# Kernel optimization log

Measured on AMD Instinct MI355X. Metric: run time of the kernel, lower is better.

## Reference

```python
import jax, jax.numpy as jnp
import numpy as np

B, N, E, K = 4, 40000, 240000, 128
C_IN, C_W, C_OUT, N_BLOCK = 6, 128, 3, 4


def setup_inputs() -> dict:
    key = jax.random.key(0)
    ks = jax.random.split(key, 20)
    s = lambda k, sh, fan: jax.random.normal(k, sh, jnp.float32) / np.sqrt(fan).astype(np.float32)
    inp = {}
    inp["x_in"] = jax.random.normal(ks[0], (B, N, C_IN), jnp.float32)
    inp["mass"] = jax.random.uniform(ks[1], (B, N), jnp.float32) + 0.1  # positive lumped mass
    inp["evals"] = jax.random.uniform(ks[2], (B, K), jnp.float32) * 10.0  # nonneg Laplacian eigenvalues
    inp["evecs"] = jax.random.normal(ks[3], (B, N, K), jnp.float32) / np.float32(np.sqrt(N))
    inp["rows"] = jax.random.randint(ks[4], (E,), 0, N, jnp.int32)
    inp["cols"] = jax.random.randint(ks[5], (E,), 0, N, jnp.int32)
    inp["gradX_vals"] = jax.random.normal(ks[6], (B, E), jnp.float32)
    inp["gradY_vals"] = jax.random.normal(ks[7], (B, E), jnp.float32)
    inp["w_first"] = s(ks[8], (C_IN, C_W), C_IN)
    inp["b_first"] = jnp.zeros((C_W,), jnp.float32)
    inp["diff_time"] = jax.random.uniform(ks[9], (N_BLOCK, C_W), jnp.float32) * 0.1 + 1e-4  # learned times, clamped positive
    inp["A_re"] = s(ks[10], (N_BLOCK, C_W, C_W), C_W)
    inp["A_im"] = s(ks[11], (N_BLOCK, C_W, C_W), C_W)
    inp["mlp_w0"] = s(ks[12], (N_BLOCK, 3 * C_W, C_W), 3 * C_W)
    inp["mlp_b0"] = jnp.zeros((N_BLOCK, C_W), jnp.float32)
    inp["mlp_w1"] = s(ks[13], (N_BLOCK, C_W, C_W), C_W)
    inp["mlp_b1"] = jnp.zeros((N_BLOCK, C_W), jnp.float32)
    inp["mlp_w2"] = s(ks[14], (N_BLOCK, C_W, C_W), C_W)
    inp["mlp_b2"] = jnp.zeros((N_BLOCK, C_W), jnp.float32)
    inp["w_last"] = s(ks[15], (C_W, C_OUT), C_W)
    inp["b_last"] = jnp.zeros((C_OUT,), jnp.float32)
    return inp


def reference(x_in, mass, evals, evecs, rows, cols, gradX_vals, gradY_vals,
              w_first, b_first, diff_time, A_re, A_im,
              mlp_w0, mlp_b0, mlp_w1, mlp_b1, mlp_w2, mlp_b2, w_last, b_last):
    def spmm(vals, x):
        # sparse [N,N] COO (shared pattern, per-sample vals) @ dense [N,C]
        return jax.ops.segment_sum(vals[:, None] * x[cols], rows, num_segments=N)

    x = x_in @ w_first + b_first  # [B,N,C_W]
    for i in range(N_BLOCK):
        # --- LearnedTimeDiffusion (spectral) ---
        x_spec = jnp.einsum('bnk,bnc->bkc', evecs, x * mass[..., None])  # [B,K,C]
        coefs = jnp.exp(-evals[:, :, None] * diff_time[i][None, None, :])  # [B,K,C]
        x_diffuse = jnp.einsum('bnk,bkc->bnc', evecs, coefs * x_spec)  # [B,N,C]
        # --- per-sample sparse gradient operators (the batched torch.mm loop) ---
        gX = jax.vmap(spmm)(gradX_vals, x_diffuse)  # [B,N,C]
        gY = jax.vmap(spmm)(gradY_vals, x_diffuse)  # [B,N,C]
        # --- SpatialGradientFeatures with learned rotations (complex multiply) ---
        Breal = gX @ A_re[i] - gY @ A_im[i]
        Bimag = gY @ A_re[i] + gX @ A_im[i]
        grad_feat = jnp.tanh(gX * Breal + gY * Bimag)  # [B,N,C]
        # --- MiniMLP + residual ---
        feat = jnp.concatenate([x, x_diffuse, grad_feat], axis=-1)  # [B,N,3C]
        h = jax.nn.relu(feat @ mlp_w0[i] + mlp_b0[i])
        h = jax.nn.relu(h @ mlp_w1[i] + mlp_b1[i])
        h = h @ mlp_w2[i] + mlp_b2[i]
        x = h + x
    return x @ w_last + b_last  # [B,N,C_OUT]
```

## Files before the change

### kernel.cpp

```cpp
#include <hip/hip_runtime.h>

#define B_ 4
#define N_ 40000
#define E_ 240000
#define NB_SCAN ((N_ + 255) / 256)

typedef unsigned short u16;
typedef unsigned int u32;
typedef __attribute__((ext_vector_type(8))) short bf16x8;
typedef __attribute__((ext_vector_type(4))) float f32x4;

__device__ __forceinline__ float b2f(u16 h) {
    u32 u = ((u32)h) << 16;
    return __uint_as_float(u);
}
__device__ __forceinline__ u16 f2b(float f) {
    u32 u = __float_as_uint(f);
    u32 r = (u + 0x7fffu + ((u >> 16) & 1u)) >> 16;
    return (u16)r;
}

__global__ __launch_bounds__(256) void first_linear_kern(
    const float* __restrict__ x_in, const float* __restrict__ w,
    const float* __restrict__ bias, u16* __restrict__ xout, int M)
{
    __shared__ float sw[6 * 128];
    __shared__ float sb[128];
    int t = threadIdx.x;
    for (int i = t; i < 768; i += 256) sw[i] = w[i];
    if (t < 128) sb[t] = bias[t];
    __syncthreads();
    int idx = blockIdx.x * 256 + t;
    int row = idx >> 4;
    int cg = (idx & 15) * 8;
    if (row >= M) return;
    const float* xr = x_in + (size_t)row * 6;
    float xv[6];
#pragma unroll
    for (int j = 0; j < 6; j++) xv[j] = xr[j];
    float acc[8];
#pragma unroll
    for (int i = 0; i < 8; i++) acc[i] = sb[cg + i];
#pragma unroll
    for (int j = 0; j < 6; j++)
#pragma unroll
        for (int i = 0; i < 8; i++) acc[i] += xv[j] * sw[j * 128 + cg + i];
    ushort4 h0, h1;
    h0.x = f2b(acc[0]); h0.y = f2b(acc[1]); h0.z = f2b(acc[2]); h0.w = f2b(acc[3]);
    h1.x = f2b(acc[4]); h1.y = f2b(acc[5]); h1.z = f2b(acc[6]); h1.w = f2b(acc[7]);
    uint4 pk;
    pk.x = (u32)h0.x | ((u32)h0.y << 16);
    pk.y = (u32)h0.z | ((u32)h0.w << 16);
    pk.z = (u32)h1.x | ((u32)h1.y << 16);
    pk.w = (u32)h1.z | ((u32)h1.w << 16);
    *(uint4*)(xout + (size_t)row * 128 + cg) = pk;
}

__global__ __launch_bounds__(256) void pack_w_kern(
    const float* __restrict__ src, u16* __restrict__ dst, int K)
{
    int i = blockIdx.z;
    src += (size_t)i * K * 128;
    dst += (size_t)i * K * 128;
    int idx = blockIdx.x * 256 + threadIdx.x;
    int n = idx / K;
    int k = idx % K;
    dst[idx] = f2b(src[(size_t)k * 128 + n]);
}

__global__ __launch_bounds__(256) void pack_rot_kern(
    const float* __restrict__ Are, const float* __restrict__ Aim,
    u16* __restrict__ WR1, u16* __restrict__ WR2)
{
    int i = blockIdx.z;
    const float* are = Are + (size_t)i * 16384;
    const float* aim = Aim + (size_t)i * 16384;
    int idx = blockIdx.x * 256 + threadIdx.x;
    int n = idx >> 8;
    int k = idx & 255;
    float v1, v2;
    if (k < 128) { float a = are[(size_t)k * 128 + n]; v1 = a; v2 = a; }
    else         { float a = aim[(size_t)(k - 128) * 128 + n]; v1 = -a; v2 = a; }
    WR1[(size_t)i * 32768 + idx] = f2b(v1);
    WR2[(size_t)i * 32768 + idx] = f2b(v2);
}

__global__ __launch_bounds__(256) void hist_kern(const int* __restrict__ rows, int* count)
{
    int e = blockIdx.x * 256 + threadIdx.x;
    if (e < E_) atomicAdd(&count[rows[e]], 1);
}

__device__ __forceinline__ int block_incl_scan_256(int v, int t)
{
    __shared__ int wsum[4];
    int lane = t & 63;
    int wid = t >> 6;
    int x = v;
#pragma unroll
    for (int off = 1; off < 64; off <<= 1) {
        int y = __shfl_up(x, off);
        if (lane >= off) x += y;
    }
    if (lane == 63) wsum[wid] = x;
    __syncthreads();
    if (t == 0) {
        int s = 0;
#pragma unroll
        for (int i = 0; i < 4; i++) { int tm = wsum[i]; wsum[i] = s; s += tm; }
    }
    __syncthreads();
    return x + wsum[wid];
}

__global__ __launch_bounds__(256) void scan1_kern(
    const int* __restrict__ count, int* __restrict__ excl_out,
    int* __restrict__ blockTotals)
{
    int t = threadIdx.x;
    int g = blockIdx.x * 256 + t;
    int v = (g < N_) ? count[g] : 0;
    int incl = block_incl_scan_256(v, t);
    if (g < N_) excl_out[g] = incl - v;
    if (t == 255) blockTotals[blockIdx.x] = incl;
}

__global__ __launch_bounds__(256) void scan2_kern(
    const int* __restrict__ blockTotals, int* __restrict__ blockOffs,
    int* __restrict__ totalOut)
{
    int t = threadIdx.x;
    int v = (t < NB_SCAN) ? blockTotals[t] : 0;
    int incl = block_incl_scan_256(v, t);
    if (t < NB_SCAN) blockOffs[t] = incl - v;
    if (t == 255) *totalOut = incl;
}

__global__ __launch_bounds__(256) void scan3_kern(
    int* __restrict__ rowptr, int* __restrict__ nextp,
    const int* __restrict__ blockOffs)
{
    int t = threadIdx.x;
    int g = blockIdx.x * 256 + t;
    if (g >= N_) return;
    int v = rowptr[g] + blockOffs[blockIdx.x];
    rowptr[g] = v;
    nextp[g] = v;
}

__global__ __launch_bounds__(256) void scatter_idx_kern(
    const int* __restrict__ rows, const int* __restrict__ cols,
    int* nextp, int* __restrict__ scols, int* __restrict__ sperm)
{
    int e = blockIdx.x * 256 + threadIdx.x;
    if (e >= E_) return;
    int r = rows[e];
    int pos = atomicAdd(&nextp[r], 1);
    scols[pos] = cols[e];
    sperm[pos] = e;
}

__global__ __launch_bounds__(256) void gather_vals_kern(
    const int* __restrict__ sperm,
    const float* __restrict__ gvx, const float* __restrict__ gvy,
    float* __restrict__ svx, float* __restrict__ svy)
{
    int pos = blockIdx.x * 256 + threadIdx.x;
    if (pos >= E_) return;
    int e = sperm[pos];
#pragma unroll
    for (int b = 0; b < B_; b++) {
        svx[(size_t)b * E_ + pos] = gvx[(size_t)b * E_ + e];
        svy[(size_t)b * E_ + pos] = gvy[(size_t)b * E_ + e];
    }
}

__global__ __launch_bounds__(256) void spmm_csr_kern(
    const int* __restrict__ rowptr, const int* __restrict__ scols,
    const float* __restrict__ svx, const float* __restrict__ svy,
    const u16* __restrict__ xd, u16* __restrict__ gXY0, u16* __restrict__ gXY1)
{
    const size_t NZ = (size_t)N_ * 128;
    int z = blockIdx.z;
    const float* svx_b = svx + (size_t)z * E_;
    const float* svy_b = svy + (size_t)z * E_;
    const u16* xd_b = xd + (size_t)z * NZ;
    u16* base = (z < 2) ? (gXY0 + (size_t)z * 2 * NZ) : (gXY1 + (size_t)(z - 2) * 2 * NZ);
    u16* gXh = base;
    u16* gYh = base + NZ;

    int t = threadIdx.x;
    int r = blockIdx.x * 4 + (t >> 6);
    int c2 = (t & 63) * 2;
    int beg = rowptr[r], end = rowptr[r + 1];
    float ax0 = 0.f, ax1 = 0.f, ay0 = 0.f, ay1 = 0.f;
    int j = beg;
    for (; j + 1 < end; j += 2) {
        int ca = scols[j], cb = scols[j + 1];
        u32 xwa = *(const u32*)(xd_b + (size_t)ca * 128 + c2);
        u32 xwb = *(const u32*)(xd_b + (size_t)cb * 128 + c2);
        float vxa = svx_b[j], vya = svy_b[j];
        float vxb = svx_b[j + 1], vyb = svy_b[j + 1];
        float xa0 = b2f((u16)(xwa & 0xffffu)), xa1 = b2f((u16)(xwa >> 16));
        float xb0 = b2f((u16)(xwb & 0xffffu)), xb1 = b2f((u16)(xwb >> 16));
        ax0 += vxa * xa0; ax1 += vxa * xa1;
        ay0 += vya * xa0; ay1 += vya * xa1;
        ax0 += vxb * xb0; ax1 += vxb * xb1;
        ay0 += vyb * xb0; ay1 += vyb * xb1;
    }
    if (j < end) {
        int col = scols[j];
        u32 xw = *(const u32*)(xd_b + (size_t)col * 128 + c2);
        float x0 = b2f((u16)(xw & 0xffffu));
        float x1 = b2f((u16)(xw >> 16));
        float vx = svx_b[j], vy = svy_b[j];
        ax0 += vx * x0; ax1 += vx * x1;
        ay0 += vy * x0; ay1 += vy * x1;
    }
    u32 px = (u32)f2b(ax0) | ((u32)f2b(ax1) << 16);
    u32 py = (u32)f2b(ay0) | ((u32)f2b(ay1) << 16);
    *(u32*)(gXh + (size_t)r * 128 + c2) = px;
    *(u32*)(gYh + (size_t)r * 128 + c2) = py;
}

__global__ __launch_bounds__(256) void spec_stage1_mfma_kern(
    const u16* __restrict__ x, const float* __restrict__ mass,
    const float* __restrict__ evecs, float* __restrict__ partials)
{
    __shared__ __align__(16) u16 sEVh[128][40];
    __shared__ __align__(16) u16 sEVl[128][40];
    __shared__ __align__(16) u16 sXM[128][40];
    int b = blockIdx.y;
    int pb = blockIdx.x;
    const u16* xb = x + (size_t)b * N_ * 128;
    const float* mb = mass + (size_t)b * N_;
    const float* eb = evecs + (size_t)b * N_ * 128;
    float* dst = partials + ((size_t)b * 128 + pb) * 16384;

    int t = threadIdx.x;
    int wv = t >> 6;
    int lane = t & 63;
    int quad = lane >> 4;
    int r16 = lane & 15;
    int kb = wv * 32;
    int kc = (t & 63) * 2;
    int nh = wv;

    f32x4 acc[2][8];
#pragma unroll
    for (int i = 0; i < 2; i++)
#pragma unroll
        for (int j = 0; j < 8; j++) acc[i][j] = (f32x4){0.f, 0.f, 0.f, 0.f};

    for (int ch = pb; ch < N_ / 32; ch += 128) {
        int nbase = ch * 32 + nh * 8;
        float4 m0 = *(const float4*)(mb + nbase);
        float4 m1 = *(const float4*)(mb + nbase + 4);
        float mm[8] = {m0.x, m0.y, m0.z, m0.w, m1.x, m1.y, m1.z, m1.w};
        u32 eh0[4], eh1[4], el0[4], el1[4], xq0[4], xq1[4];
#pragma unroll
        for (int jp = 0; jp < 4; jp++) {
            eh0[jp] = 0; eh1[jp] = 0; el0[jp] = 0;
            el1[jp] = 0; xq0[jp] = 0; xq1[jp] = 0;
        }
#pragma unroll
        for (int j = 0; j < 8; j++) {
            float2 e = *(const float2*)(eb + (size_t)(nbase + j) * 128 + kc);
            u32 xw = *(const u32*)(xb + (size_t)(nbase + j) * 128 + kc);
            u16 h0 = f2b(e.x);
            u16 h1 = f2b(e.y);
            u16 l0 = f2b(e.x - b2f(h0));
            u16 l1 = f2b(e.y - b2f(h1));
            u16 q0 = f2b(b2f((u16)(xw & 0xffffu)) * mm[j]);
            u16 q1 = f2b(b2f((u16)(xw >> 16)) * mm[j]);
            int sh = (j & 1) * 16;
            int jp = j >> 1;
            eh0[jp] |= ((u32)h0) << sh; eh1[jp] |= ((u32)h1) << sh;
            el0[jp] |= ((u32)l0) << sh; el1[jp] |= ((u32)l1) << sh;
            xq0[jp] |= ((u32)q0) << sh; xq1[jp] |= ((u32)q1) << sh;
        }
        __syncthreads();
        *(uint4*)&sEVh[kc][nh * 8]     = make_uint4(eh0[0], eh0[1], eh0[2], eh0[3]);
        *(uint4*)&sEVh[kc + 1][nh * 8] = make_uint4(eh1[0], eh1[1], eh1[2], eh1[3]);
        *(uint4*)&sEVl[kc][nh * 8]     = make_uint4(el0[0], el0[1], el0[2], el0[3]);
        *(uint4*)&sEVl[kc + 1][nh * 8] = make_uint4(el1[0], el1[1], el1[2], el1[3]);
        *(uint4*)&sXM[kc][nh * 8]      = make_uint4(xq0[0], xq0[1], xq0[2], xq0[3]);
        *(uint4*)&sXM[kc + 1][nh * 8]  = make_uint4(xq1[0], xq1[1], xq1[2], xq1[3]);
        __syncthreads();

        bf16x8 ah0 = *(const bf16x8*)&sEVh[kb + r16][quad * 8];
        bf16x8 ah1 = *(const bf16x8*)&sEVh[kb + 16 + r16][quad * 8];
        bf16x8 al0 = *(const bf16x8*)&sEVl[kb + r16][quad * 8];
        bf16x8 al1 = *(const bf16x8*)&sEVl[kb + 16 + r16][quad * 8];
#pragma unroll
        for (int nt = 0; nt < 8; nt++) {
            bf16x8 bx = *(const bf16x8*)&sXM[nt * 16 + r16][quad * 8];
            acc[0][nt] = __builtin_amdgcn_mfma_f32_16x16x32_bf16(ah0, bx, acc[0][nt], 0, 0, 0);
            acc[1][nt] = __builtin_amdgcn_mfma_f32_16x16x32_bf16(ah1, bx, acc[1][nt], 0, 0, 0);
            acc[0][nt] = __builtin_amdgcn_mfma_f32_16x16x32_bf16(al0, bx, acc[0][nt], 0, 0, 0);
            acc[1][nt] = __builtin_amdgcn_mfma_f32_16x16x32_bf16(al1, bx, acc[1][nt], 0, 0, 0);
        }
    }

#pragma unroll
    for (int mt = 0; mt < 2; mt++)
#pragma unroll
        for (int nt = 0; nt < 8; nt++)
#pragma unroll
            for (int reg = 0; reg < 4; reg++) {
                int kk = kb + mt * 16 + quad * 4 + reg;
                int cc = nt * 16 + r16;
                dst[(size_t)kk * 128 + cc] = acc[mt][nt][reg];
            }
}

__global__ __launch_bounds__(128) void spec_stage2_coef_kern(
    const float* __restrict__ partials, const float* __restrict__ evals,
    const float* __restrict__ dt, u16* __restrict__ ys_t)
{
    int b = blockIdx.x >> 7;
    int k = blockIdx.x & 127;
    int c = threadIdx.x;
    const float* p = partials + (size_t)b * 128 * 16384 + (size_t)k * 128 + c;
    float s = 0.f;
#pragma unroll 8
    for (int pb = 0; pb < 128; pb++) s += p[(size_t)pb * 16384];
    float co = expf(-evals[b * 128 + k] * dt[c]);
    ys_t[((size_t)b * 128 + c) * 128 + k] = f2b(s * co);
}

template <int KK, bool AF32>
__global__ __launch_bounds__(256) void mgemm_kern(
    const void* __restrict__ A0v,
    const u16* __restrict__ Wp, u16* __restrict__ outp,
    size_t aBatch, size_t wBatch, size_t oBatch)
{
    __shared__ u16 sA[64][72];
    __shared__ u16 sB[128][72];
    int z = blockIdx.z;
    const u16* Wb = Wp + wBatch * (size_t)z;
    size_t aOff = aBatch * (size_t)z;
    size_t oOff = oBatch * (size_t)z;

    int t = threadIdx.x;
    int m0 = blockIdx.x * 64;
    int wv = t >> 6;
    int lane = t & 63;
    int quad = lane >> 4;
    int r16 = lane & 15;
    int mw = (wv & 1) * 32;
    int nw = (wv >> 1) * 64;

    f32x4 acc[2][4];
#pragma unroll
    for (int i = 0; i < 2; i++)
#pragma unroll
        for (int j = 0; j < 4; j++) acc[i][j] = (f32x4){0.f, 0.f, 0.f, 0.f};

#pragma unroll 1
    for (int kt = 0; kt < KK / 64; kt++) {
        int kbase = kt * 64;
        __syncthreads();
        if (AF32) {
            const float* Af = (const float*)A0v + aOff;
#pragma unroll
            for (int p = 0; p < 4; p++) {
                int idx = p * 256 + t;
                int row = idx >> 4;
                int seg = idx & 15;
                float4 v = *(const float4*)(Af + (size_t)(m0 + row) * 128 + kbase + seg * 4);
                ushort4 h;
                h.x = f2b(v.x); h.y = f2b(v.y); h.z = f2b(v.z); h.w = f2b(v.w);
                *(ushort4*)&sA[row][seg * 4] = h;
            }
        } else {
            const u16* Ah = (const u16*)A0v + aOff;
#pragma unroll
            for (int p = 0; p < 2; p++) {
                int idx = p * 256 + t;
                int row = idx >> 3;
                int seg = idx & 7;
                *(uint4*)&sA[row][seg * 8] =
                    *(const uint4*)(Ah + (size_t)(m0 + row) * 128 + kbase + seg * 8);
            }
        }
        {
#pragma unroll
            for (int p = 0; p < 4; p++) {
                int idx = p * 256 + t;
                int n = idx >> 3;
                int seg = idx & 7;
                *(uint4*)&sB[n][seg * 8] =
                    *(const uint4*)(Wb + (size_t)n * KK + kbase + seg * 8);
            }
        }
        __syncthreads();

#pragma unroll
        for (int ks = 0; ks < 2; ks++) {
            int ko = ks * 32 + quad * 8;
            bf16x8 a0 = *(const bf16x8*)&sA[mw + r16][ko];
            bf16x8 a1 = *(const bf16x8*)&sA[mw + 16 + r16][ko];
            bf16x8 b0 = *(const bf16x8*)&sB[nw + r16][ko];
            bf16x8 b1 = *(const bf16x8*)&sB[nw + 16 + r16][ko];
            bf16x8 b2 = *(const bf16x8*)&sB[nw + 32 + r16][ko];
            bf16x8 b3 = *(const bf16x8*)&sB[nw + 48 + r16][ko];
            acc[0][0] = __builtin_amdgcn_mfma_f32_16x16x32_bf16(a0, b0, acc[0][0], 0, 0, 0);
            acc[0][1] = __builtin_amdgcn_mfma_f32_16x16x32_bf16(a0, b1, acc[0][1], 0, 0, 0);
            acc[0][2] = __builtin_amdgcn_mfma_f32_16x16x32_bf16(a0, b2, acc[0][2], 0, 0, 0);
            acc[0][3] = __builtin_amdgcn_mfma_f32_16x16x32_bf16(a0, b3, acc[0][3], 0, 0, 0);
            acc[1][0] = __builtin_amdgcn_mfma_f32_16x16x32_bf16(a1, b0, acc[1][0], 0, 0, 0);
            acc[1][1] = __builtin_amdgcn_mfma_f32_16x16x32_bf16(a1, b1, acc[1][1], 0, 0, 0);
            acc[1][2] = __builtin_amdgcn_mfma_f32_16x16x32_bf16(a1, b2, acc[1][2], 0, 0, 0);
            acc[1][3] = __builtin_amdgcn_mfma_f32_16x16x32_bf16(a1, b3, acc[1][3], 0, 0, 0);
        }
    }

#pragma unroll
    for (int nt = 0; nt < 4; nt++) {
        int col = nw + nt * 16 + r16;
#pragma unroll
        for (int mt = 0; mt < 2; mt++) {
#pragma unroll
            for (int reg = 0; reg < 4; reg++) {
                int row = m0 + mw + mt * 16 + quad * 4 + reg;
                outp[oOff + (size_t)row * 128 + col] = f2b(acc[mt][nt][reg]);
            }
        }
    }
}

__global__ __launch_bounds__(512) void mlp_rot_fused_kern(
    const u16* __restrict__ xg, const u16* __restrict__ xdg,
    const u16* __restrict__ gXY0, const u16* __restrict__ gXY1,
    const u16* __restrict__ WR1, const u16* __restrict__ WR2,
    const u16* __restrict__ W0, const u16* __restrict__ W1, const u16* __restrict__ W2,
    const float* __restrict__ b0, const float* __restrict__ b1, const float* __restrict__ b2,
    u16* __restrict__ outp)
{
    __shared__ u16 sGX[64][136];
    __shared__ u16 sGY[64][136];
    __shared__ u16 sB[128][72];
    __shared__ __align__(16) u16 sHbuf[9728];
    __shared__ u16 sA[64][72];
#define HV(r, c) sHbuf[(r) * 152 + (c)]
#define WV(n, c) sHbuf[(n) * 72 + (c)]

    const size_t NZ = (size_t)N_ * 128;
    int z = blockIdx.z;
    const u16* gX = (z < 2) ? (gXY0 + (size_t)z * 2 * NZ) : (gXY1 + (size_t)(z - 2) * 2 * NZ);
    const u16* gY = gX + NZ;
    int m0n = blockIdx.x * 64;
    size_t growBase = ((size_t)z * N_ + m0n) * 128;

    int t = threadIdx.x;
    int wv = t >> 6;
    int lane = t & 63;
    int quad = lane >> 4;
    int r16 = lane & 15;
    int mw = (wv & 1) * 32;
    int nw = (wv >> 1) * 32;

#pragma unroll
    for (int p = 0; p < 2; p++) {
        int idx = p * 512 + t;
        int row = idx >> 4;
        int seg = idx & 15;
        *(uint4*)&sGX[row][seg * 8] = *(const uint4*)(gX + (size_t)(m0n + row) * 128 + seg * 8);
        *(uint4*)&sGY[row][seg * 8] = *(const uint4*)(gY + (size_t)(m0n + row) * 128 + seg * 8);
    }

    f32x4 accRe[2][2], accIm[2][2];
#pragma unroll
    for (int i = 0; i < 2; i++)
#pragma unroll
        for (int j = 0; j < 2; j++) {
            accRe[i][j] = (f32x4){0.f, 0.f, 0.f, 0.f};
            accIm[i][j] = (f32x4){0.f, 0.f, 0.f, 0.f};
        }

#pragma unroll 1
    for (int c = 0; c < 4; c++) {
        __syncthreads();
#pragma unroll
        for (int p = 0; p < 2; p++) {
            int idx = p * 512 + t;
            int n = idx >> 3;
            int seg = idx & 7;
            *(uint4*)&sB[n][seg * 8] = *(const uint4*)(WR1 + (size_t)n * 256 + c * 64 + seg * 8);
            *(uint4*)&WV(n, seg * 8) = *(const uint4*)(WR2 + (size_t)n * 256 + c * 64 + seg * 8);
        }
        __syncthreads();

        const u16 (*sRe)[136] = (c < 2) ? sGX : sGY;
        const u16 (*sIm)[136] = (c < 2) ? sGY : sGX;
        int kob = (c & 1) * 64;
#pragma unroll
        for (int ks = 0; ks < 2; ks++) {
            int ko = kob + ks * 32 + quad * 8;
            int kb = ks * 32 + quad * 8;
            bf16x8 aRe0 = *(const bf16x8*)&sRe[mw + r16][ko];
            bf16x8 aRe1 = *(const bf16x8*)&sRe[mw + 16 + r16][ko];
            bf16x8 aIm0 = *(const bf16x8*)&sIm[mw + r16][ko];
            bf16x8 aIm1 = *(const bf16x8*)&sIm[mw + 16 + r16][ko];
#pragma unroll
            for (int j = 0; j < 2; j++) {
                bf16x8 w1f = *(const bf16x8*)&sB[nw + 16 * j + r16][kb];
                bf16x8 w2f = *(const bf16x8*)&WV(nw + 16 * j + r16, kb);
                accRe[0][j] = __builtin_amdgcn_mfma_f32_16x16x32_bf16(aRe0, w1f, accRe[0][j], 0, 0, 0);
                accRe[1][j] = __builtin_amdgcn_mfma_f32_16x16x32_bf16(aRe1, w1f, accRe[1][j], 0, 0, 0);
                accIm[0][j] = __builtin_amdgcn_mfma_f32_16x16x32_bf16(aIm0, w2f, accIm[0][j], 0, 0, 0);
                accIm[1][j] = __builtin_amdgcn_mfma_f32_16x16x32_bf16(aIm1, w2f, accIm[1][j], 0, 0, 0);
            }
        }
    }

    __syncthreads();
#pragma unroll
    for (int nt = 0; nt < 2; nt++) {
        int col = nw + nt * 16 + r16;
#pragma unroll
        for (int mt = 0; mt < 2; mt++)
#pragma unroll
            for (int reg = 0; reg < 4; reg++) {
                int lrow = mw + mt * 16 + quad * 4 + reg;
                float gx = b2f(sGX[lrow][col]);
                float gy = b2f(sGY[lrow][col]);
                float v = tanhf(gx * accRe[mt][nt][reg] + gy * accIm[mt][nt][reg]);
                sGX[lrow][col] = f2b(v);
            }
    }

    f32x4 acc[2][2];
#pragma unroll
    for (int i = 0; i < 2; i++)
#pragma unroll
        for (int j = 0; j < 2; j++) acc[i][j] = (f32x4){0.f, 0.f, 0.f, 0.f};
#pragma unroll 1
    for (int kt = 0; kt < 6; kt++) {
        int kbase = kt * 64;
        int kloc = kbase & 127;
        __syncthreads();
        if (kt < 4) {
            const u16* Ap = (kt < 2) ? xg : xdg;
            {
                int row = t >> 3;
                int seg = t & 7;
                *(uint4*)&sA[row][seg * 8] =
                    *(const uint4*)(Ap + growBase + (size_t)row * 128 + kloc + seg * 8);
            }
        }
#pragma unroll
        for (int p = 0; p < 2; p++) {
            int idx = p * 512 + t;
            int n = idx >> 3;
            int seg = idx & 7;
            *(uint4*)&sB[n][seg * 8] = *(const uint4*)(W0 + (size_t)n * 384 + kbase + seg * 8);
        }
        __syncthreads();
#pragma unroll
        for (int ks = 0; ks < 2; ks++) {
            int ko = ks * 32 + quad * 8;
            bf16x8 a0, a1;
            if (kt < 4) {
                a0 = *(const bf16x8*)&sA[mw + r16][ko];
                a1 = *(const bf16x8*)&sA[mw + 16 + r16][ko];
            } else {
                a0 = *(const bf16x8*)&sGX[mw + r16][kloc + ko];
                a1 = *(const bf16x8*)&sGX[mw + 16 + r16][kloc + ko];
            }
#pragma unroll
            for (int j = 0; j < 2; j++) {
                bf16x8 bj = *(const bf16x8*)&sB[nw + 16 * j + r16][ko];
                acc[0][j] = __builtin_amdgcn_mfma_f32_16x16x32_bf16(a0, bj, acc[0][j], 0, 0, 0);
                acc[1][j] = __builtin_amdgcn_mfma_f32_16x16x32_bf16(a1, bj, acc[1][j], 0, 0, 0);
            }
        }
    }
    __syncthreads();
#pragma unroll
    for (int nt = 0; nt < 2; nt++) {
        int col = nw + nt * 16 + r16;
        float bv = b0[col];
#pragma unroll
        for (int mt = 0; mt < 2; mt++)
#pragma unroll
            for (int reg = 0; reg < 4; reg++) {
                int rl = mw + mt * 16 + quad * 4 + reg;
                HV(rl, col) = f2b(fmaxf(acc[mt][nt][reg] + bv, 0.f));
            }
    }

#pragma unroll
    for (int i = 0; i < 2; i++)
#pragma unroll
        for (int j = 0; j < 2; j++) acc[i][j] = (f32x4){0.f, 0.f, 0.f, 0.f};
#pragma unroll 1
    for (int kt = 0; kt < 2; kt++) {
        int kbase = kt * 64;
        __syncthreads();
#pragma unroll
        for (int p = 0; p < 2; p++) {
            int idx = p * 512 + t;
            int n = idx >> 3;
            int seg = idx & 7;
            *(uint4*)&sB[n][seg * 8] = *(const uint4*)(W1 + (size_t)n * 128 + kbase + seg * 8);
        }
        __syncthreads();
#pragma unroll
        for (int ks = 0; ks < 2; ks++) {
            int ko = kbase + ks * 32 + quad * 8;
            int kb = ks * 32 + quad * 8;
            bf16x8 a0 = *(const bf16x8*)&HV(mw + r16, ko);
            bf16x8 a1 = *(const bf16x8*)&HV(mw + 16 + r16, ko);
#pragma unroll
            for (int j = 0; j < 2; j++) {
                bf16x8 bj = *(const bf16x8*)&sB[nw + 16 * j + r16][kb];
                acc[0][j] = __builtin_amdgcn_mfma_f32_16x16x32_bf16(a0, bj, acc[0][j], 0, 0, 0);
                acc[1][j] = __builtin_amdgcn_mfma_f32_16x16x32_bf16(a1, bj, acc[1][j], 0, 0, 0);
            }
        }
    }
    __syncthreads();
#pragma unroll
    for (int nt = 0; nt < 2; nt++) {
        int col = nw + nt * 16 + r16;
        float bv = b1[col];
#pragma unroll
        for (int mt = 0; mt < 2; mt++)
#pragma unroll
            for (int reg = 0; reg < 4; reg++) {
                int rl = mw + mt * 16 + quad * 4 + reg;
                HV(rl, col) = f2b(fmaxf(acc[mt][nt][reg] + bv, 0.f));
            }
    }

#pragma unroll
    for (int i = 0; i < 2; i++)
#pragma unroll
        for (int j = 0; j < 2; j++) acc[i][j] = (f32x4){0.f, 0.f, 0.f, 0.f};
#pragma unroll 1
    for (int kt = 0; kt < 2; kt++) {
        int kbase = kt * 64;
        __syncthreads();
#pragma unroll
        for (int p = 0; p < 2; p++) {
            int idx = p * 512 + t;
            int n = idx >> 3;
            int seg = idx & 7;
            *(uint4*)&sB[n][seg * 8] = *(const uint4*)(W2 + (size_t)n * 128 + kbase + seg * 8);
        }
        __syncthreads();
#pragma unroll
        for (int ks = 0; ks < 2; ks++) {
            int ko = kbase + ks * 32 + quad * 8;
            int kb = ks * 32 + quad * 8;
            bf16x8 a0 = *(const bf16x8*)&HV(mw + r16, ko);
            bf16x8 a1 = *(const bf16x8*)&HV(mw + 16 + r16, ko);
#pragma unroll
            for (int j = 0; j < 2; j++) {
                bf16x8 bj = *(const bf16x8*)&sB[nw + 16 * j + r16][kb];
                acc[0][j] = __builtin_amdgcn_mfma_f32_16x16x32_bf16(a0, bj, acc[0][j], 0, 0, 0);
                acc[1][j] = __builtin_amdgcn_mfma_f32_16x16x32_bf16(a1, bj, acc[1][j], 0, 0, 0);
            }
        }
    }
#pragma unroll
    for (int nt = 0; nt < 2; nt++) {
        int col = nw + nt * 16 + r16;
        float bv = b2[col];
#pragma unroll
        for (int mt = 0; mt < 2; mt++)
#pragma unroll
            for (int reg = 0; reg < 4; reg++) {
                int row = mw + mt * 16 + quad * 4 + reg;
                float v = acc[mt][nt][reg] + bv + b2f(xg[growBase + (size_t)row * 128 + col]);
                outp[growBase + (size_t)row * 128 + col] = f2b(v);
            }
    }
#undef HV
#undef WV
}

__global__ __launch_bounds__(256) void last_linear_kern(
    const u16* __restrict__ x, const float* __restrict__ w,
    const float* __restrict__ bias, float* __restrict__ outp, int M)
{
    __shared__ float sw[128 * 3];
    int t = threadIdx.x;
    for (int i = t; i < 384; i += 256) sw[i] = w[i];
    __syncthreads();
    int wave = t >> 6;
    int lane = t & 63;
    int row = blockIdx.x * 4 + wave;
    if (row >= M) return;
    const u16* xr = x + (size_t)row * 128;
    float p0 = 0.f, p1 = 0.f, p2 = 0.f;
#pragma unroll
    for (int h = 0; h < 2; h++) {
        int c = lane + h * 64;
        float xv = b2f(xr[c]);
        p0 += xv * sw[c * 3 + 0];
        p1 += xv * sw[c * 3 + 1];
        p2 += xv * sw[c * 3 + 2];
    }
#pragma unroll
    for (int off = 32; off > 0; off >>= 1) {
        p0 += __shfl_xor(p0, off);
        p1 += __shfl_xor(p1, off);
        p2 += __shfl_xor(p2, off);
    }
    if (lane == 0) {
        float* o = outp + (size_t)row * 3;
        o[0] = p0 + bias[0];
        o[1] = p1 + bias[1];
        o[2] = p2 + bias[2];
    }
}

extern "C" void kernel_launch(void* const* d_in, const int* in_sizes, int n_in,
                              void* d_out, int out_size, void* d_ws, size_t ws_size,
                              hipStream_t stream)
{
    const float* x_in    = (const float*)d_in[0];
    const float* mass    = (const float*)d_in[1];
    const float* evals   = (const float*)d_in[2];
    const float* evecs   = (const float*)d_in[3];
    const int*   rows    = (const int*)  d_in[4];
    const int*   cols    = (const int*)  d_in[5];
    const float* gvx     = (const float*)d_in[6];
    const float* gvy     = (const float*)d_in[7];
    const float* w_first = (const float*)d_in[8];
    const float* b_first = (const float*)d_in[9];
    const float* dtimes  = (const float*)d_in[10];
    const float* A_re    = (const float*)d_in[11];
    const float* A_im    = (const float*)d_in[12];
    const float* w0      = (const float*)d_in[13];
    const float* b0      = (const float*)d_in[14];
    const float* w1      = (const float*)d_in[15];
    const float* b1      = (const float*)d_in[16];
    const float* w2      = (const float*)d_in[17];
    const float* b2      = (const float*)d_in[18];
    const float* w_last  = (const float*)d_in[19];
    const float* b_last  = (const float*)d_in[20];
    float* outp = (float*)d_out;

    const size_t SZ = (size_t)B_ * N_ * 128;
    const size_t NZ = (size_t)N_ * 128;

    u16* P0 = (u16*)d_ws;
    u16* P1 = P0 + SZ;
    u16* GF = P1 + SZ;
    float* SC = (float*)(GF + SZ);
    u16* ys_t = (u16*)(SC + 8388608);
    u16* WP0 = (u16*)(SC + 2 * NZ);
    u16* WP1 = WP0 + 4 * 49152;
    u16* WP2 = WP1 + 4 * 16384;
    u16* WR1 = WP2 + 4 * 16384;
    u16* WR2 = WR1 + 4 * 32768;
    int* rowptr = (int*)(WR2 + 4 * 32768);
    int* nextp  = rowptr + 40004;
    int* scols  = nextp + N_;
    float* svx  = (float*)(scols + E_);
    float* svy  = svx + (size_t)B_ * E_;

    u16* x  = P0;
    u16* xd = P1;
    const int M = B_ * N_;

    int* bTot  = (int*)SC;
    int* bOff  = bTot + 512;
    int* sperm = bTot + 1024;
    hipMemsetAsync(nextp, 0, N_ * sizeof(int), stream);
    hist_kern<<<dim3((E_ + 255) / 256), 256, 0, stream>>>(rows, nextp);
    scan1_kern<<<dim3(NB_SCAN), 256, 0, stream>>>(nextp, rowptr, bTot);
    scan2_kern<<<dim3(1), 256, 0, stream>>>(bTot, bOff, rowptr + N_);
    scan3_kern<<<dim3(NB_SCAN), 256, 0, stream>>>(rowptr, nextp, bOff);
    scatter_idx_kern<<<dim3((E_ + 255) / 256), 256, 0, stream>>>(
        rows, cols, nextp, scols, sperm);
    gather_vals_kern<<<dim3((E_ + 255) / 256), 256, 0, stream>>>(
        sperm, gvx, gvy, svx, svy);

    pack_w_kern<<<dim3(192, 1, 4), 256, 0, stream>>>(w0, WP0, 384);
    pack_w_kern<<<dim3(64, 1, 4), 256, 0, stream>>>(w1, WP1, 128);
    pack_w_kern<<<dim3(64, 1, 4), 256, 0, stream>>>(w2, WP2, 128);
    pack_rot_kern<<<dim3(128, 1, 4), 256, 0, stream>>>(A_re, A_im, WR1, WR2);

    first_linear_kern<<<dim3(M * 16 / 256), 256, 0, stream>>>(x_in, w_first, b_first, x, M);

    u16* GXY0 = GF;
    u16* GXY1 = (u16*)SC;

    for (int i = 0; i < 4; i++) {
        spec_stage1_mfma_kern<<<dim3(128, B_), 256, 0, stream>>>(x, mass, evecs, SC);
        spec_stage2_coef_kern<<<dim3(B_ * 128), 128, 0, stream>>>(
            SC, evals, dtimes + (size_t)i * 128, ys_t);
        mgemm_kern<128, true><<<dim3(N_ / 64, 1, B_), 256, 0, stream>>>(
            evecs, ys_t, xd, NZ, (size_t)128 * 128, NZ);
        spmm_csr_kern<<<dim3(N_ / 4, 1, B_), 256, 0, stream>>>(
            rowptr, scols, svx, svy, xd, GXY0, GXY1);
        mlp_rot_fused_kern<<<dim3(N_ / 64, 1, B_), 512, 0, stream>>>(
            x, xd, GXY0, GXY1,
            WR1 + (size_t)i * 32768, WR2 + (size_t)i * 32768,
            WP0 + (size_t)i * 49152, WP1 + (size_t)i * 16384, WP2 + (size_t)i * 16384,
            b0 + (size_t)i * 128, b1 + (size_t)i * 128, b2 + (size_t)i * 128,
            xd);
        u16* tmp = x; x = xd; xd = tmp;
    }

    last_linear_kern<<<dim3(M / 4), 256, 0, stream>>>(x, w_last, b_last, outp, M);
}
```

Before: 1.209 ms.

## Load MFMA operands directly from global memory instead of staging through LDS

The diffuse GEMM and the fused rotation/MLP kernel now feed MFMA fragments straight from global memory (evecs converted to bf16 in registers, weights read per lane). This drops the shared-memory staging and most of the block-wide barriers. Shared memory use falls to the gradient tiles plus one hidden buffer, which may raise occupancy. The cost is uncoalesced, redundant global reads of the weight and activation fragments that now depend on L1/L2 hits.

Result: slower. 1.681 ms (+39.1%).

```diff
diff --git a/kernel.cpp b/kernel.cpp
--- a/kernel.cpp
+++ b/kernel.cpp
@@ -18,6 +18,14 @@
     u32 u = __float_as_uint(f);
     u32 r = (u + 0x7fffu + ((u >> 16) & 1u)) >> 16;
     return (u16)r;
+}
+__device__ __forceinline__ bf16x8 ld8f(const float* p) {
+    float4 v0 = *(const float4*)p;
+    float4 v1 = *(const float4*)(p + 4);
+    union { bf16x8 v; u16 s[8]; } u;
+    u.s[0] = f2b(v0.x); u.s[1] = f2b(v0.y); u.s[2] = f2b(v0.z); u.s[3] = f2b(v0.w);
+    u.s[4] = f2b(v1.x); u.s[5] = f2b(v1.y); u.s[6] = f2b(v1.z); u.s[7] = f2b(v1.w);
+    return u.v;
 }
 
 __global__ __launch_bounds__(256) void first_linear_kern(
@@ -329,18 +337,15 @@
     ys_t[((size_t)b * 128 + c) * 128 + k] = f2b(s * co);
 }
 
-template <int KK, bool AF32>
-__global__ __launch_bounds__(256) void mgemm_kern(
-    const void* __restrict__ A0v,
-    const u16* __restrict__ Wp, u16* __restrict__ outp,
-    size_t aBatch, size_t wBatch, size_t oBatch)
-{
-    __shared__ u16 sA[64][72];
-    __shared__ u16 sB[128][72];
+__global__ __launch_bounds__(256) void diffuse_gemm_kern(
+    const float* __restrict__ evecs, const u16* __restrict__ ys_t,
+    u16* __restrict__ xd)
+{
+    const size_t NZ = (size_t)N_ * 128;
     int z = blockIdx.z;
-    const u16* Wb = Wp + wBatch * (size_t)z;
-    size_t aOff = aBatch * (size_t)z;
-    size_t oOff = oBatch * (size_t)z;
+    const float* eb = evecs + (size_t)z * NZ;
+    const u16* yb = ys_t + (size_t)z * 16384;
+    u16* ob = xd + (size_t)z * NZ;
 
     int t = threadIdx.x;
     int m0 = blockIdx.x * 64;
@@ -357,62 +362,25 @@
 #pragma unroll
         for (int j = 0; j < 4; j++) acc[i][j] = (f32x4){0.f, 0.f, 0.f, 0.f};
 
-#pragma unroll 1
-    for (int kt = 0; kt < KK / 64; kt++) {
-        int kbase = kt * 64;
-        __syncthreads();
-        if (AF32) {
-            const float* Af = (const float*)A0v + aOff;
-#pragma unroll
-            for (int p = 0; p < 4; p++) {
-                int idx = p * 256 + t;
-                int row = idx >> 4;
-                int seg = idx & 15;
-                float4 v = *(const float4*)(Af + (size_t)(m0 + row) * 128 + kbase + seg * 4);
-                ushort4 h;
-                h.x = f2b(v.x); h.y = f2b(v.y); h.z = f2b(v.z); h.w = f2b(v.w);
-                *(ushort4*)&sA[row][seg * 4] = h;
-            }
-        } else {
-            const u16* Ah = (const u16*)A0v + aOff;
-#pragma unroll
-            for (int p = 0; p < 2; p++) {
-                int idx = p * 256 + t;
-                int row = idx >> 3;
-                int seg = idx & 7;
-                *(uint4*)&sA[row][seg * 8] =
-                    *(const uint4*)(Ah + (size_t)(m0 + row) * 128 + kbase + seg * 8);
-            }
-        }
-        {
-#pragma unroll
-            for (int p = 0; p < 4; p++) {
-                int idx = p * 256 + t;
-                int n = idx >> 3;
-                int seg = idx & 7;
-                *(uint4*)&sB[n][seg * 8] =
-                    *(const uint4*)(Wb + (size_t)n * KK + kbase + seg * 8);
-            }
-        }
-        __syncthreads();
-
+#pragma unroll
+    for (int kt = 0; kt < 2; kt++) {
 #pragma unroll
         for (int ks = 0; ks < 2; ks++) {
-            int ko = ks * 32 + quad * 8;
-            bf16x8 a0 = *(const bf16x8*)&sA[mw + r16][ko];
-            bf16x8 a1 = *(const bf16x8*)&sA[mw + 16 + r16][ko];
-            bf16x8 b0 = *(const bf16x8*)&sB[nw + r16][ko];
-            bf16x8 b1 = *(const bf16x8*)&sB[nw + 16 + r16][ko];
-            bf16x8 b2 = *(const bf16x8*)&sB[nw + 32 + r16][ko];
-            bf16x8 b3 = *(const bf16x8*)&sB[nw + 48 + r16][ko];
+            int ko = kt * 64 + ks * 32 + quad * 8;
+            bf16x8 a0 = ld8f(eb + (size_t)(m0 + mw + r16) * 128 + ko);
+            bf16x8 a1 = ld8f(eb + (size_t)(m0 + mw + 16 + r16) * 128 + ko);
+            bf16x8 b0 = *(const bf16x8*)(yb + (size_t)(nw + r16) * 128 + ko);
+            bf16x8 b1 = *(const bf16x8*)(yb + (size_t)(nw + 16 + r16) * 128 + ko);
+            bf16x8 b2v = *(const bf16x8*)(yb + (size_t)(nw + 32 + r16) * 128 + ko);
+            bf16x8 b3v = *(const bf16x8*)(yb + (size_t)(nw + 48 + r16) * 128 + ko);
             acc[0][0] = __builtin_amdgcn_mfma_f32_16x16x32_bf16(a0, b0, acc[0][0], 0, 0, 0);
             acc[0][1] = __builtin_amdgcn_mfma_f32_16x16x32_bf16(a0, b1, acc[0][1], 0, 0, 0);
-            acc[0][2] = __builtin_amdgcn_mfma_f32_16x16x32_bf16(a0, b2, acc[0][2], 0, 0, 0);
-            acc[0][3] = __builtin_amdgcn_mfma_f32_16x16x32_bf16(a0, b3, acc[0][3], 0, 0, 0);
+            acc[0][2] = __builtin_amdgcn_mfma_f32_16x16x32_bf16(a0, b2v, acc[0][2], 0, 0, 0);
+            acc[0][3] = __builtin_amdgcn_mfma_f32_16x16x32_bf16(a0, b3v, acc[0][3], 0, 0, 0);
             acc[1][0] = __builtin_amdgcn_mfma_f32_16x16x32_bf16(a1, b0, acc[1][0], 0, 0, 0);
             acc[1][1] = __builtin_amdgcn_mfma_f32_16x16x32_bf16(a1, b1, acc[1][1], 0, 0, 0);
-            acc[1][2] = __builtin_amdgcn_mfma_f32_16x16x32_bf16(a1, b2, acc[1][2], 0, 0, 0);
-            acc[1][3] = __builtin_amdgcn_mfma_f32_16x16x32_bf16(a1, b3, acc[1][3], 0, 0, 0);
+            acc[1][2] = __builtin_amdgcn_mfma_f32_16x16x32_bf16(a1, b2v, acc[1][2], 0, 0, 0);
+            acc[1][3] = __builtin_amdgcn_mfma_f32_16x16x32_bf16(a1, b3v, acc[1][3], 0, 0, 0);
         }
     }
 
@@ -424,7 +392,7 @@
 #pragma unroll
             for (int reg = 0; reg < 4; reg++) {
                 int row = m0 + mw + mt * 16 + quad * 4 + reg;
-                outp[oOff + (size_t)row * 128 + col] = f2b(acc[mt][nt][reg]);
+                ob[(size_t)row * 128 + col] = f2b(acc[mt][nt][reg]);
             }
         }
     }
@@ -440,11 +408,7 @@
 {
     __shared__ u16 sGX[64][136];
     __shared__ u16 sGY[64][136];
-    __shared__ u16 sB[128][72];
-    __shared__ __align__(16) u16 sHbuf[9728];
-    __shared__ u16 sA[64][72];
-#define HV(r, c) sHbuf[(r) * 152 + (c)]
-#define WV(n, c) sHbuf[(n) * 72 + (c)]
+    __shared__ u16 sH[64][136];
 
     const size_t NZ = (size_t)N_ * 128;
     int z = blockIdx.z;
@@ -469,6 +433,7 @@
         *(uint4*)&sGX[row][seg * 8] = *(const uint4*)(gX + (size_t)(m0n + row) * 128 + seg * 8);
         *(uint4*)&sGY[row][seg * 8] = *(const uint4*)(gY + (size_t)(m0n + row) * 128 + seg * 8);
     }
+    __syncthreads();
 
     f32x4 accRe[2][2], accIm[2][2];
 #pragma unroll
@@ -479,34 +444,24 @@
             accIm[i][j] = (f32x4){0.f, 0.f, 0.f, 0.f};
         }
 
-#pragma unroll 1
+#pragma unroll
     for (int c = 0; c < 4; c++) {
-        __syncthreads();
-#pragma unroll
-        for (int p = 0; p < 2; p++) {
-            int idx = p * 512 + t;
-            int n = idx >> 3;
-            int seg = idx & 7;
-            *(uint4*)&sB[n][seg * 8] = *(const uint4*)(WR1 + (size_t)n * 256 + c * 64 + seg * 8);
-            *(uint4*)&WV(n, seg * 8) = *(const uint4*)(WR2 + (size_t)n * 256 + c * 64 + seg * 8);
-        }
-        __syncthreads();
-
         const u16 (*sRe)[136] = (c < 2) ? sGX : sGY;
         const u16 (*sIm)[136] = (c < 2) ? sGY : sGX;
         int kob = (c & 1) * 64;
 #pragma unroll
         for (int ks = 0; ks < 2; ks++) {
             int ko = kob + ks * 32 + quad * 8;
-            int kb = ks * 32 + quad * 8;
+            int wk = c * 64 + ks * 32 + quad * 8;
             bf16x8 aRe0 = *(const bf16x8*)&sRe[mw + r16][ko];
             bf16x8 aRe1 = *(const bf16x8*)&sRe[mw + 16 + r16][ko];
             bf16x8 aIm0 = *(const bf16x8*)&sIm[mw + r16][ko];
             bf16x8 aIm1 = *(const bf16x8*)&sIm[mw + 16 + r16][ko];
 #pragma unroll
             for (int j = 0; j < 2; j++) {
-                bf16x8 w1f = *(const bf16x8*)&sB[nw + 16 * j + r16][kb];
-                bf16x8 w2f = *(const bf16x8*)&WV(nw + 16 * j + r16, kb);
+                int n = nw + 16 * j + r16;
+                bf16x8 w1f = *(const bf16x8*)(WR1 + (size_t)n * 256 + wk);
+                bf16x8 w2f = *(const bf16x8*)(WR2 + (size_t)n * 256 + wk);
                 accRe[0][j] = __builtin_amdgcn_mfma_f32_16x16x32_bf16(aRe0, w1f, accRe[0][j], 0, 0, 0);
                 accRe[1][j] = __builtin_amdgcn_mfma_f32_16x16x32_bf16(aRe1, w1f, accRe[1][j], 0, 0, 0);
                 accIm[0][j] = __builtin_amdgcn_mfma_f32_16x16x32_bf16(aIm0, w2f, accIm[0][j], 0, 0, 0);
@@ -530,54 +485,38 @@
                 sGX[lrow][col] = f2b(v);
             }
     }
+    __syncthreads();
 
     f32x4 acc[2][2];
 #pragma unroll
     for (int i = 0; i < 2; i++)
 #pragma unroll
         for (int j = 0; j < 2; j++) acc[i][j] = (f32x4){0.f, 0.f, 0.f, 0.f};
-#pragma unroll 1
+#pragma unroll
     for (int kt = 0; kt < 6; kt++) {
         int kbase = kt * 64;
         int kloc = kbase & 127;
-        __syncthreads();
-        if (kt < 4) {
-            const u16* Ap = (kt < 2) ? xg : xdg;
-            {
-                int row = t >> 3;
-                int seg = t & 7;
-                *(uint4*)&sA[row][seg * 8] =
-                    *(const uint4*)(Ap + growBase + (size_t)row * 128 + kloc + seg * 8);
-            }
-        }
-#pragma unroll
-        for (int p = 0; p < 2; p++) {
-            int idx = p * 512 + t;
-            int n = idx >> 3;
-            int seg = idx & 7;
-            *(uint4*)&sB[n][seg * 8] = *(const uint4*)(W0 + (size_t)n * 384 + kbase + seg * 8);
-        }
-        __syncthreads();
 #pragma unroll
         for (int ks = 0; ks < 2; ks++) {
             int ko = ks * 32 + quad * 8;
             bf16x8 a0, a1;
             if (kt < 4) {
-                a0 = *(const bf16x8*)&sA[mw + r16][ko];
-                a1 = *(const bf16x8*)&sA[mw + 16 + r16][ko];
+                const u16* Ap = (kt < 2) ? xg : xdg;
+                a0 = *(const bf16x8*)(Ap + growBase + (size_t)(mw + r16) * 128 + kloc + ko);
+                a1 = *(const bf16x8*)(Ap + growBase + (size_t)(mw + 16 + r16) * 128 + kloc + ko);
             } else {
                 a0 = *(const bf16x8*)&sGX[mw + r16][kloc + ko];
                 a1 = *(const bf16x8*)&sGX[mw + 16 + r16][kloc + ko];
             }
 #pragma unroll
             for (int j = 0; j < 2; j++) {
-                bf16x8 bj = *(const bf16x8*)&sB[nw + 16 * j + r16][ko];
+                int n = nw + 16 * j + r16;
+                bf16x8 bj = *(const bf16x8*)(W0 + (size_t)n * 384 + kbase + ko);
                 acc[0][j] = __builtin_amdgcn_mfma_f32_16x16x32_bf16(a0, bj, acc[0][j], 0, 0, 0);
                 acc[1][j] = __builtin_amdgcn_mfma_f32_16x16x32_bf16(a1, bj, acc[1][j], 0, 0, 0);
             }
         }
     }
-    __syncthreads();
 #pragma unroll
     for (int nt = 0; nt < 2; nt++) {
         int col = nw + nt * 16 + r16;
@@ -587,35 +526,26 @@
 #pragma unroll
             for (int reg = 0; reg < 4; reg++) {
                 int rl = mw + mt * 16 + quad * 4 + reg;
-                HV(rl, col) = f2b(fmaxf(acc[mt][nt][reg] + bv, 0.f));
-            }
-    }
+                sH[rl][col] = f2b(fmaxf(acc[mt][nt][reg] + bv, 0.f));
+            }
+    }
+    __syncthreads();
 
 #pragma unroll
     for (int i = 0; i < 2; i++)
 #pragma unroll
         for (int j = 0; j < 2; j++) acc[i][j] = (f32x4){0.f, 0.f, 0.f, 0.f};
-#pragma unroll 1
+#pragma unroll
     for (int kt = 0; kt < 2; kt++) {
-        int kbase = kt * 64;
-        __syncthreads();
-#pragma unroll
-        for (int p = 0; p < 2; p++) {
-            int idx = p * 512 + t;
-            int n = idx >> 3;
-            int seg = idx & 7;
-            *(uint4*)&sB[n][seg * 8] = *(const uint4*)(W1 + (size_t)n * 128 + kbase + seg * 8);
-        }
-        __syncthreads();
 #pragma unroll
         for (int ks = 0; ks < 2; ks++) {
-            int ko = kbase + ks * 32 + quad * 8;
-            int kb = ks * 32 + quad * 8;
-            bf16x8 a0 = *(const bf16x8*)&HV(mw + r16, ko);
-            bf16x8 a1 = *(const bf16x8*)&HV(mw + 16 + r16, ko);
+            int ko = kt * 64 + ks * 32 + quad * 8;
+            bf16x8 a0 = *(const bf16x8*)&sH[mw + r16][ko];
+            bf16x8 a1 = *(const bf16x8*)&sH[mw + 16 + r16][ko];
 #pragma unroll
             for (int j = 0; j < 2; j++) {
-                bf16x8 bj = *(const bf16x8*)&sB[nw + 16 * j + r16][kb];
+                int n = nw + 16 * j + r16;
+                bf16x8 bj = *(const bf16x8*)(W1 + (size_t)n * 128 + ko);
                 acc[0][j] = __builtin_amdgcn_mfma_f32_16x16x32_bf16(a0, bj, acc[0][j], 0, 0, 0);
                 acc[1][j] = __builtin_amdgcn_mfma_f32_16x16x32_bf16(a1, bj, acc[1][j], 0, 0, 0);
             }
@@ -631,35 +561,26 @@
 #pragma unroll
             for (int reg = 0; reg < 4; reg++) {
                 int rl = mw + mt * 16 + quad * 4 + reg;
-                HV(rl, col) = f2b(fmaxf(acc[mt][nt][reg] + bv, 0.f));
-            }
-    }
+                sH[rl][col] = f2b(fmaxf(acc[mt][nt][reg] + bv, 0.f));
+            }
+    }
+    __syncthreads();
 
 #pragma unroll
     for (int i = 0; i < 2; i++)
 #pragma unroll
         for (int j = 0; j < 2; j++) acc[i][j] = (f32x4){0.f, 0.f, 0.f, 0.f};
-#pragma unroll 1
+#pragma unroll
     for (int kt = 0; kt < 2; kt++) {
-        int kbase = kt * 64;
-        __syncthreads();
-#pragma unroll
-        for (int p = 0; p < 2; p++) {
-            int idx = p * 512 + t;
-            int n = idx >> 3;
-            int seg = idx & 7;
-            *(uint4*)&sB[n][seg * 8] = *(const uint4*)(W2 + (size_t)n * 128 + kbase + seg * 8);
-        }
-        __syncthreads();
 #pragma unroll
         for (int ks = 0; ks < 2; ks++) {
-            int ko = kbase + ks * 32 + quad * 8;
-            int kb = ks * 32 + quad * 8;
-            bf16x8 a0 = *(const bf16x8*)&HV(mw + r16, ko);
-            bf16x8 a1 = *(const bf16x8*)&HV(mw + 16 + r16, ko);
+            int ko = kt * 64 + ks * 32 + quad * 8;
+            bf16x8 a0 = *(const bf16x8*)&sH[mw + r16][ko];
+            bf16x8 a1 = *(const bf16x8*)&sH[mw + 16 + r16][ko];
 #pragma unroll
             for (int j = 0; j < 2; j++) {
-                bf16x8 bj = *(const bf16x8*)&sB[nw + 16 * j + r16][kb];
+                int n = nw + 16 * j + r16;
+                bf16x8 bj = *(const bf16x8*)(W2 + (size_t)n * 128 + ko);
                 acc[0][j] = __builtin_amdgcn_mfma_f32_16x16x32_bf16(a0, bj, acc[0][j], 0, 0, 0);
                 acc[1][j] = __builtin_amdgcn_mfma_f32_16x16x32_bf16(a1, bj, acc[1][j], 0, 0, 0);
             }
@@ -678,8 +599,6 @@
                 outp[growBase + (size_t)row * 128 + col] = f2b(v);
             }
     }
-#undef HV
-#undef WV
 }
 
 __global__ __launch_bounds__(256) void last_linear_kern(
@@ -795,8 +714,7 @@
         spec_stage1_mfma_kern<<<dim3(128, B_), 256, 0, stream>>>(x, mass, evecs, SC);
         spec_stage2_coef_kern<<<dim3(B_ * 128), 128, 0, stream>>>(
             SC, evals, dtimes + (size_t)i * 128, ys_t);
-        mgemm_kern<128, true><<<dim3(N_ / 64, 1, B_), 256, 0, stream>>>(
-            evecs, ys_t, xd, NZ, (size_t)128 * 128, NZ);
+        diffuse_gemm_kern<<<dim3(N_ / 64, 1, B_), 256, 0, stream>>>(evecs, ys_t, xd);
         spmm_csr_kern<<<dim3(N_ / 4, 1, B_), 256, 0, stream>>>(
             rowptr, scols, svx, svy, xd, GXY0, GXY1);
         mlp_rot_fused_kern<<<dim3(N_ / 64, 1, B_), 512, 0, stream>>>(
```

## Register-prefetch weight tiles in fused MLP kernel, split stage2 reduction, fast tanh

Applied to the files above, without the earlier changes.

In the fused rotation/MLP kernel, the next K-slice of the weight and activation tiles is now loaded into registers while the current slice is being consumed. This hides global-load latency behind the MFMA work across the rotation, W0, W1 and W2 phases. The spectral stage-2 reduction is split across four thread groups per block with a shared-memory combine, giving more parallel loads. tanhf is replaced by an exp-based fast_tanh with clamping, which costs a little accuracy and holds more registers live.

Measured after the change: 1.173 ms. -3.0%, faster.

```diff
diff --git a/kernel.cpp b/kernel.cpp
--- a/kernel.cpp
+++ b/kernel.cpp
@@ -18,6 +18,11 @@
     u32 u = __float_as_uint(f);
     u32 r = (u + 0x7fffu + ((u >> 16) & 1u)) >> 16;
     return (u16)r;
+}
+__device__ __forceinline__ float fast_tanh(float x) {
+    float cx = fminf(fmaxf(x, -9.f), 9.f);
+    float e = __expf(2.f * cx);
+    return (e - 1.f) / (e + 1.f);
 }
 
 __global__ __launch_bounds__(256) void first_linear_kern(
@@ -314,19 +319,26 @@
             }
 }
 
-__global__ __launch_bounds__(128) void spec_stage2_coef_kern(
+__global__ __launch_bounds__(512) void spec_stage2_coef_kern(
     const float* __restrict__ partials, const float* __restrict__ evals,
     const float* __restrict__ dt, u16* __restrict__ ys_t)
 {
+    __shared__ float red[4][128];
     int b = blockIdx.x >> 7;
     int k = blockIdx.x & 127;
-    int c = threadIdx.x;
+    int c = threadIdx.x & 127;
+    int g = threadIdx.x >> 7;
     const float* p = partials + (size_t)b * 128 * 16384 + (size_t)k * 128 + c;
     float s = 0.f;
 #pragma unroll 8
-    for (int pb = 0; pb < 128; pb++) s += p[(size_t)pb * 16384];
-    float co = expf(-evals[b * 128 + k] * dt[c]);
-    ys_t[((size_t)b * 128 + c) * 128 + k] = f2b(s * co);
+    for (int pb = g; pb < 128; pb += 4) s += p[(size_t)pb * 16384];
+    red[g][c] = s;
+    __syncthreads();
+    if (g == 0) {
+        float tot = (red[0][c] + red[1][c]) + (red[2][c] + red[3][c]);
+        float co = expf(-evals[b * 128 + k] * dt[c]);
+        ys_t[((size_t)b * 128 + c) * 128 + k] = f2b(tot * co);
+    }
 }
 
 template <int KK, bool AF32>
@@ -461,6 +473,18 @@
     int mw = (wv & 1) * 32;
     int nw = (wv >> 1) * 32;
 
+    int n8 = t >> 3;
+    int sg8 = (t & 7) * 8;
+
+    const u16* w1base  = WR1 + (size_t)n8 * 256 + sg8;
+    const u16* w1base2 = WR1 + (size_t)(n8 + 64) * 256 + sg8;
+    const u16* w2base  = WR2 + (size_t)n8 * 256 + sg8;
+    const u16* w2base2 = WR2 + (size_t)(n8 + 64) * 256 + sg8;
+    uint4 r1a = *(const uint4*)(w1base);
+    uint4 r1b = *(const uint4*)(w1base2);
+    uint4 r2a = *(const uint4*)(w2base);
+    uint4 r2b = *(const uint4*)(w2base2);
+
 #pragma unroll
     for (int p = 0; p < 2; p++) {
         int idx = p * 512 + t;
@@ -482,13 +506,15 @@
 #pragma unroll 1
     for (int c = 0; c < 4; c++) {
         __syncthreads();
-#pragma unroll
-        for (int p = 0; p < 2; p++) {
-            int idx = p * 512 + t;
-            int n = idx >> 3;
-            int seg = idx & 7;
-            *(uint4*)&sB[n][seg * 8] = *(const uint4*)(WR1 + (size_t)n * 256 + c * 64 + seg * 8);
-            *(uint4*)&WV(n, seg * 8) = *(const uint4*)(WR2 + (size_t)n * 256 + c * 64 + seg * 8);
+        *(uint4*)&sB[n8][sg8]      = r1a;
+        *(uint4*)&sB[n8 + 64][sg8] = r1b;
+        *(uint4*)&WV(n8, sg8)      = r2a;
+        *(uint4*)&WV(n8 + 64, sg8) = r2b;
+        if (c < 3) {
+            r1a = *(const uint4*)(w1base  + (c + 1) * 64);
+            r1b = *(const uint4*)(w1base2 + (c + 1) * 64);
+            r2a = *(const uint4*)(w2base  + (c + 1) * 64);
+            r2b = *(const uint4*)(w2base2 + (c + 1) * 64);
         }
         __syncthreads();
 
@@ -515,6 +541,14 @@
         }
     }
 
+    const u16* w0base  = W0 + (size_t)n8 * 384 + sg8;
+    const u16* w0base2 = W0 + (size_t)(n8 + 64) * 384 + sg8;
+    const u16* xbase  = xg  + growBase + (size_t)n8 * 128 + sg8;
+    const u16* xdbase = xdg + growBase + (size_t)n8 * 128 + sg8;
+    uint4 rB0 = *(const uint4*)(w0base);
+    uint4 rB1 = *(const uint4*)(w0base2);
+    uint4 rA  = *(const uint4*)(xbase);
+
     __syncthreads();
 #pragma unroll
     for (int nt = 0; nt < 2; nt++) {
@@ -526,7 +560,7 @@
                 int lrow = mw + mt * 16 + quad * 4 + reg;
                 float gx = b2f(sGX[lrow][col]);
                 float gy = b2f(sGY[lrow][col]);
-                float v = tanhf(gx * accRe[mt][nt][reg] + gy * accIm[mt][nt][reg]);
+                float v = fast_tanh(gx * accRe[mt][nt][reg] + gy * accIm[mt][nt][reg]);
                 sGX[lrow][col] = f2b(v);
             }
     }
@@ -538,24 +572,21 @@
         for (int j = 0; j < 2; j++) acc[i][j] = (f32x4){0.f, 0.f, 0.f, 0.f};
 #pragma unroll 1
     for (int kt = 0; kt < 6; kt++) {
-        int kbase = kt * 64;
-        int kloc = kbase & 127;
-        __syncthreads();
-        if (kt < 4) {
-            const u16* Ap = (kt < 2) ? xg : xdg;
-            {
-                int row = t >> 3;
-                int seg = t & 7;
-                *(uint4*)&sA[row][seg * 8] =
-                    *(const uint4*)(Ap + growBase + (size_t)row * 128 + kloc + seg * 8);
-            }
-        }
-#pragma unroll
-        for (int p = 0; p < 2; p++) {
-            int idx = p * 512 + t;
-            int n = idx >> 3;
-            int seg = idx & 7;
-            *(uint4*)&sB[n][seg * 8] = *(const uint4*)(W0 + (size_t)n * 384 + kbase + seg * 8);
+        int kloc = (kt * 64) & 127;
+        __syncthreads();
+        if (kt < 4) *(uint4*)&sA[n8][sg8] = rA;
+        *(uint4*)&sB[n8][sg8]      = rB0;
+        *(uint4*)&sB[n8 + 64][sg8] = rB1;
+        if (kt < 5) {
+            rB0 = *(const uint4*)(w0base  + (kt + 1) * 64);
+            rB1 = *(const uint4*)(w0base2 + (kt + 1) * 64);
+        } else {
+            rB0 = *(const uint4*)(W1 + (size_t)n8 * 128 + sg8);
+            rB1 = *(const uint4*)(W1 + (size_t)(n8 + 64) * 128 + sg8);
+        }
+        if (kt < 3) {
+            const u16* nbp = (kt + 1 < 2) ? xbase : xdbase;
+            rA = *(const uint4*)(nbp + (((kt + 1) * 64) & 127));
         }
         __syncthreads();
 #pragma unroll
@@ -597,19 +628,20 @@
         for (int j = 0; j < 2; j++) acc[i][j] = (f32x4){0.f, 0.f, 0.f, 0.f};
 #pragma unroll 1
     for (int kt = 0; kt < 2; kt++) {
-        int kbase = kt * 64;
-        __syncthreads();
-#pragma unroll
-        for (int p = 0; p < 2; p++) {
-            int idx = p * 512 + t;
-            int n = idx >> 3;
-            int seg = idx & 7;
-            *(uint4*)&sB[n][seg * 8] = *(const uint4*)(W1 + (size_t)n * 128 + kbase + seg * 8);
+        __syncthreads();
+        *(uint4*)&sB[n8][sg8]      = rB0;
+        *(uint4*)&sB[n8 + 64][sg8] = rB1;
+        if (kt == 0) {
+            rB0 = *(const uint4*)(W1 + (size_t)n8 * 128 + 64 + sg8);
+            rB1 = *(const uint4*)(W1 + (size_t)(n8 + 64) * 128 + 64 + sg8);
+        } else {
+            rB0 = *(const uint4*)(W2 + (size_t)n8 * 128 + sg8);
+            rB1 = *(const uint4*)(W2 + (size_t)(n8 + 64) * 128 + sg8);
         }
         __syncthreads();
 #pragma unroll
         for (int ks = 0; ks < 2; ks++) {
-            int ko = kbase + ks * 32 + quad * 8;
+            int ko = kt * 64 + ks * 32 + quad * 8;
             int kb = ks * 32 + quad * 8;
             bf16x8 a0 = *(const bf16x8*)&HV(mw + r16, ko);
             bf16x8 a1 = *(const bf16x8*)&HV(mw + 16 + r16, ko);
@@ -641,19 +673,17 @@
         for (int j = 0; j < 2; j++) acc[i][j] = (f32x4){0.f, 0.f, 0.f, 0.f};
 #pragma unroll 1
     for (int kt = 0; kt < 2; kt++) {
-        int kbase = kt * 64;
-        __syncthreads();
-#pragma unroll
-        for (int p = 0; p < 2; p++) {
-            int idx = p * 512 + t;
-            int n = idx >> 3;
-            int seg = idx & 7;
-            *(uint4*)&sB[n][seg * 8] = *(const uint4*)(W2 + (size_t)n * 128 + kbase + seg * 8);
+        __syncthreads();
+        *(uint4*)&sB[n8][sg8]      = rB0;
+        *(uint4*)&sB[n8 + 64][sg8] = rB1;
+        if (kt == 0) {
+            rB0 = *(const uint4*)(W2 + (size_t)n8 * 128 + 64 + sg8);
+            rB1 = *(const uint4*)(W2 + (size_t)(n8 + 64) * 128 + 64 + sg8);
         }
         __syncthreads();
 #pragma unroll
         for (int ks = 0; ks < 2; ks++) {
-            int ko = kbase + ks * 32 + quad * 8;
+            int ko = kt * 64 + ks * 32 + quad * 8;
             int kb = ks * 32 + quad * 8;
             bf16x8 a0 = *(const bf16x8*)&HV(mw + r16, ko);
             bf16x8 a1 = *(const bf16x8*)&HV(mw + 16 + r16, ko);
@@ -793,7 +823,7 @@
 
     for (int i = 0; i < 4; i++) {
         spec_stage1_mfma_kern<<<dim3(128, B_), 256, 0, stream>>>(x, mass, evecs, SC);
-        spec_stage2_coef_kern<<<dim3(B_ * 128), 128, 0, stream>>>(
+        spec_stage2_coef_kern<<<dim3(B_ * 128), 512, 0, stream>>>(
             SC, evals, dtimes + (size_t)i * 128, ys_t);
         mgemm_kern<128, true><<<dim3(N_ / 64, 1, B_), 256, 0, stream>>>(
             evecs, ys_t, xd, NZ, (size_t)128 * 128, NZ);
```
